# Kernel optimization log

Hardware: AMD Instinct MI355X
Metric: run time of the kernel (lower is better)

## Reference

```python
import jax, jax.numpy as jnp
import numpy as np
import math

E = 1024      # hidden_dim = embed_dim (num_heads=1 so head_dim=E)
ND = 512      # output_dim = asymmetric value dim
N_DOMAIN = 2048
LN_EPS = 1e-5
SCALE = math.sqrt(1.0 / E) * 2.0 * math.log(N_DOMAIN)


def layernorm(x, g, b):
    mu = jnp.mean(x, axis=-1, keepdims=True)
    var = jnp.var(x, axis=-1, keepdims=True)
    return (x - mu) * jax.lax.rsqrt(var + LN_EPS) * g + b


def setup_inputs() -> dict:
    key = jax.random.key(0)
    ks = jax.random.split(key, 5)
    B, L = 8, 2048
    return {
        "x": jax.random.normal(ks[0], (B, L, E), dtype=jnp.float32),
        "in_proj_w": jax.random.normal(ks[1], (2 * E + ND, E), dtype=jnp.float32) * 0.02,
        "w1": jax.random.normal(ks[2], (2048, ND), dtype=jnp.float32) * 0.02,
        "b1": jnp.zeros((2048,), dtype=jnp.float32),
        "w2": jax.random.normal(ks[3], (ND, 2048), dtype=jnp.float32) * 0.02,
        "b2": jnp.zeros((ND,), dtype=jnp.float32),
        "g1": jnp.ones((ND,), dtype=jnp.float32),
        "be1": jnp.zeros((ND,), dtype=jnp.float32),
        "g2": jnp.ones((ND,), dtype=jnp.float32),
        "be2": jnp.zeros((ND,), dtype=jnp.float32),
    }


def reference(x, in_proj_w, w1, b1, w2, b2, g1, be1, g2, be2):
    # fused in-projection (no bias): q,k get E dims, v gets ND dims
    proj = jnp.einsum("ble,fe->blf", x, in_proj_w)
    q = proj[..., :E]
    k = proj[..., E:2 * E]
    v = proj[..., 2 * E:]
    # custom scale: sqrt(1/head_dim) * 2 * log(N)
    scores = jnp.einsum("bld,bsd->bls", q * SCALE, k)  # [B, L, S]
    attn_w = jax.nn.softmax(scores, axis=-1)
    attn_out = jnp.einsum("bls,bsd->bld", attn_w, v)   # [B, L, ND] (no out proj)
    # skip=False (hidden_dim != output_dim): norm1(attn) only
    h = layernorm(attn_out, g1, be1)
    ff = jnp.einsum("bld,fd->blf", h, w1) + b1
    ff = jnp.einsum("blf,df->bld", jax.nn.relu(ff), w2) + b2
    return layernorm(h + ff, g2, be2)
```

## Files before the change

### kernel.cpp

```cpp
#include <hip/hip_runtime.h>
#include <hip/hip_bf16.h>

typedef unsigned short u16;
typedef unsigned int u32;
typedef float f32x4 __attribute__((ext_vector_type(4)));
typedef _Float16 f16x8 __attribute__((ext_vector_type(8)));
typedef u32 u32x4 __attribute__((ext_vector_type(4)));
typedef u32 u32x2 __attribute__((ext_vector_type(2)));

#define SEQ 2048
#define EDIM 1024

__device__ __forceinline__ u16 f2h(float f) {
  _Float16 h = (_Float16)f;
  return __builtin_bit_cast(u16, h);
}
__device__ __forceinline__ float h2f(u16 u) {
  return (float)__builtin_bit_cast(_Float16, u);
}
__device__ __forceinline__ u32 pk(float a, float b) {
  return (u32)f2h(a) | ((u32)f2h(b) << 16);
}

__global__ __launch_bounds__(256) void cvt_f16(const float* __restrict__ in,
                                               u16* __restrict__ out, int n8) {
  int i = blockIdx.x * 256 + threadIdx.x;
  if (i >= n8) return;
  const f32x4* p = (const f32x4*)(in + (size_t)i * 8);
  f32x4 a = p[0], b = p[1];
  u32x4 o = {pk(a[0], a[1]), pk(a[2], a[3]), pk(b[0], b[1]), pk(b[2], b[3])};
  *(u32x4*)(out + (size_t)i * 8) = o;
}

struct GemmP {
  const u16* A; const u16* B;
  int lda, ldb, K;
  long bsA, bsB, bsC;
  float* Cf; int ldc;
  u16* Cb;
  const float* bias;
  const u16* resid;
  u16* qk; u16* vT;
  float scale;
};

template <int EPI>
__global__ __launch_bounds__(512, 2) void gemm256(GemmP p) {
  __shared__ __align__(16) char lds[131072];
  const int tid = threadIdx.x;
  const int lane = tid & 63;
  const int wave = tid >> 6;
  const int wm = wave >> 2, wn = wave & 3;
  const int bn0 = blockIdx.x * 256;
  const int bm0 = blockIdx.y * 256;
  const int z = blockIdx.z;
  const u16* Ab = p.A + (long)z * p.bsA + (long)bm0 * p.lda;
  const u16* Bb = p.B + (long)z * p.bsB + (long)bn0 * p.ldb;

  const int ch0 = tid, ch1 = tid + 512;
  const int r0 = ch0 >> 2, s0 = ch0 & 3;
  const int r1 = ch1 >> 2, s1 = ch1 & 3;
  const long srcA0 = (long)r0 * p.lda + ((s0 ^ ((r0 >> 1) & 3)) << 3);
  const long srcA1 = (long)r1 * p.lda + ((s1 ^ ((r1 >> 1) & 3)) << 3);
  const long srcB0 = (long)r0 * p.ldb + ((s0 ^ ((r0 >> 1) & 3)) << 3);
  const long srcB1 = (long)r1 * p.ldb + ((s1 ^ ((r1 >> 1) & 3)) << 3);

  auto stage = [&](int s) {
    const int base = (s & 3) * 32768;
    const int k0 = s * 32;
    __builtin_amdgcn_global_load_lds(
        (const __attribute__((address_space(1))) u32*)(Ab + k0 + srcA0),
        (__attribute__((address_space(3))) u32*)(lds + base + ch0 * 16), 16, 0, 0);
    __builtin_amdgcn_global_load_lds(
        (const __attribute__((address_space(1))) u32*)(Ab + k0 + srcA1),
        (__attribute__((address_space(3))) u32*)(lds + base + ch1 * 16), 16, 0, 0);
    __builtin_amdgcn_global_load_lds(
        (const __attribute__((address_space(1))) u32*)(Bb + k0 + srcB0),
        (__attribute__((address_space(3))) u32*)(lds + base + 16384 + ch0 * 16), 16, 0, 0);
    __builtin_amdgcn_global_load_lds(
        (const __attribute__((address_space(1))) u32*)(Bb + k0 + srcB1),
        (__attribute__((address_space(3))) u32*)(lds + base + 16384 + ch1 * 16), 16, 0, 0);
  };

  int aoff[8], boff[4];
#pragma unroll
  for (int m = 0; m < 8; ++m) {
    int r = wm * 128 + m * 16 + (lane & 15);
    aoff[m] = r * 64 + ((((lane >> 4)) ^ ((r >> 1) & 3)) << 4);
  }
#pragma unroll
  for (int n = 0; n < 4; ++n) {
    int r = wn * 64 + n * 16 + (lane & 15);
    boff[n] = 16384 + r * 64 + ((((lane >> 4)) ^ ((r >> 1) & 3)) << 4);
  }

  f32x4 acc[8][4] = {};

  stage(0); stage(1); stage(2);
  asm volatile("s_waitcnt vmcnt(8)" ::: "memory");
  __builtin_amdgcn_s_barrier();
  asm volatile("" ::: "memory");

  const int NS = p.K >> 5;
  for (int s = 0; s < NS; ++s) {
    if (s + 3 < NS) stage(s + 3);
    const char* base = lds + (s & 3) * 32768;
    f16x8 av[8], bv[4];
#pragma unroll
    for (int m = 0; m < 8; ++m) av[m] = *(const f16x8*)(base + aoff[m]);
#pragma unroll
    for (int n = 0; n < 4; ++n) bv[n] = *(const f16x8*)(base + boff[n]);
    __builtin_amdgcn_s_setprio(1);
#pragma unroll
    for (int m = 0; m < 8; ++m)
#pragma unroll
      for (int n = 0; n < 4; ++n)
        acc[m][n] = __builtin_amdgcn_mfma_f32_16x16x32_f16(av[m], bv[n], acc[m][n], 0, 0, 0);
    __builtin_amdgcn_s_setprio(0);
    __builtin_amdgcn_sched_barrier(0);
    if (s + 3 < NS) {
      asm volatile("s_waitcnt vmcnt(8)" ::: "memory");
    } else if (s + 2 < NS) {
      asm volatile("s_waitcnt vmcnt(4)" ::: "memory");
    } else if (s + 1 < NS) {
      asm volatile("s_waitcnt vmcnt(0)" ::: "memory");
    }
    __builtin_amdgcn_s_barrier();
    asm volatile("" ::: "memory");
  }

#pragma unroll
  for (int i = 0; i < 8; ++i) {
#pragma unroll
    for (int j = 0; j < 4; ++j) {
      int mb = bm0 + wm * 128 + i * 16 + ((lane >> 4) << 2);
      int n = bn0 + wn * 64 + j * 16 + (lane & 15);
      if constexpr (EPI == 0) {
        float* dst = p.Cf + (long)z * p.bsC + (long)mb * p.ldc + n;
#pragma unroll
        for (int r = 0; r < 4; ++r) dst[(long)r * p.ldc] = acc[i][j][r];
      } else if constexpr (EPI == 1) {
        int b = mb >> 11, l0 = mb & 2047;
        if (n < EDIM) {
          u16* dst = p.qk + (long)b * 4194304 + (long)l0 * 1024 + n;
#pragma unroll
          for (int r = 0; r < 4; ++r) dst[r * 1024] = f2h(acc[i][j][r] * p.scale);
        } else if (n < 2 * EDIM) {
          u16* dst = p.qk + (long)b * 4194304 + 2097152 + (long)l0 * 1024 + (n - EDIM);
#pragma unroll
          for (int r = 0; r < 4; ++r) dst[r * 1024] = f2h(acc[i][j][r]);
        } else {
          u16* dst = p.vT + (long)b * 1048576 + (long)(n - 2 * EDIM) * 2048 + l0;
          u32x2 w = {pk(acc[i][j][0], acc[i][j][1]), pk(acc[i][j][2], acc[i][j][3])};
          *(u32x2*)dst = w;
        }
      } else if constexpr (EPI == 2) {
        u16* dst = p.Cb + (long)mb * p.ldc + n;
        float bias = p.bias[n];
#pragma unroll
        for (int r = 0; r < 4; ++r) dst[(long)r * p.ldc] = f2h(fmaxf(acc[i][j][r] + bias, 0.f));
      }
    }
  }
}

template <int EPI>
__global__ __launch_bounds__(256) void gemm_bt(GemmP p) {
  __shared__ __align__(16) char lds[32768];
  const int tid = threadIdx.x;
  const int lane = tid & 63;
  const int wave = tid >> 6;
  const int wm = wave >> 1, wn = wave & 1;
  const int bn0 = blockIdx.x * 128;
  const int bm0 = blockIdx.y * 128;
  const int z = blockIdx.z;
  const u16* Ab = p.A + (long)z * p.bsA + (long)bm0 * p.lda;
  const u16* Bb = p.B + (long)z * p.bsB + (long)bn0 * p.ldb;

  auto stage = [&](int k0) {
#pragma unroll
    for (int i = 0; i < 4; ++i) {
      int ch = i * 256 + tid;
      int row = ch >> 3, s = ch & 7;
      int ks = ((s ^ (row & 7)) << 3);
      __builtin_amdgcn_global_load_lds(
          (const __attribute__((address_space(1))) u32*)(Ab + (long)row * p.lda + k0 + ks),
          (__attribute__((address_space(3))) u32*)(lds + ch * 16), 16, 0, 0);
    }
#pragma unroll
    for (int i = 0; i < 4; ++i) {
      int ch = i * 256 + tid;
      int row = ch >> 3, s = ch & 7;
      int ks = ((s ^ (row & 7)) << 3);
      __builtin_amdgcn_global_load_lds(
          (const __attribute__((address_space(1))) u32*)(Bb + (long)row * p.ldb + k0 + ks),
          (__attribute__((address_space(3))) u32*)(lds + 16384 + ch * 16), 16, 0, 0);
    }
  };

  f32x4 acc[4][4] = {};
  stage(0);
  const int nk = p.K >> 6;
  for (int kt = 0; kt < nk; ++kt) {
    __syncthreads();
#pragma unroll
    for (int h = 0; h < 2; ++h) {
      f16x8 av[4], bv[4];
#pragma unroll
      for (int i = 0; i < 4; ++i) {
        int row = wm * 64 + i * 16 + (lane & 15);
        int sw = ((h << 2) | (lane >> 4)) ^ (lane & 7);
        av[i] = *(const f16x8*)(lds + row * 128 + sw * 16);
      }
#pragma unroll
      for (int j = 0; j < 4; ++j) {
        int row = wn * 64 + j * 16 + (lane & 15);
        int sw = ((h << 2) | (lane >> 4)) ^ (lane & 7);
        bv[j] = *(const f16x8*)(lds + 16384 + row * 128 + sw * 16);
      }
#pragma unroll
      for (int i = 0; i < 4; ++i)
#pragma unroll
        for (int j = 0; j < 4; ++j)
          acc[i][j] = __builtin_amdgcn_mfma_f32_16x16x32_f16(av[i], bv[j], acc[i][j], 0, 0, 0);
    }
    __syncthreads();
    if (kt + 1 < nk) stage((kt + 1) << 6);
  }

#pragma unroll
  for (int i = 0; i < 4; ++i) {
#pragma unroll
    for (int j = 0; j < 4; ++j) {
      int mb = bm0 + wm * 64 + i * 16 + ((lane >> 4) << 2);
      int n = bn0 + wn * 64 + j * 16 + (lane & 15);
      if constexpr (EPI == 0) {
        float* dst = p.Cf + (long)z * p.bsC + (long)mb * p.ldc + n;
#pragma unroll
        for (int r = 0; r < 4; ++r) dst[(long)r * p.ldc] = acc[i][j][r];
      } else {
        float bias = p.bias[n];
        float* dst = p.Cf + (long)mb * 512 + n;
        const u16* rs = p.resid + (long)mb * 512 + n;
#pragma unroll
        for (int r = 0; r < 4; ++r) dst[r * 512] = acc[i][j][r] + bias + h2f(rs[r * 512]);
      }
    }
  }
}

__global__ __launch_bounds__(256) void softmax_rows(const float* __restrict__ S,
                                                    u16* __restrict__ W, int b0) {
  int r = blockIdx.x;
  int z = r >> 11, l = r & 2047;
  int tid = threadIdx.x, lane = tid & 63, wv = tid >> 6;
  const float* x = S + (long)r * 2048 + tid * 8;
  f32x4 a = *(const f32x4*)x, b = *(const f32x4*)(x + 4);
  float m = fmaxf(fmaxf(fmaxf(a[0], a[1]), fmaxf(a[2], a[3])),
                  fmaxf(fmaxf(b[0], b[1]), fmaxf(b[2], b[3])));
#pragma unroll
  for (int off = 32; off; off >>= 1) m = fmaxf(m, __shfl_xor(m, off));
  __shared__ float red[8];
  if (lane == 0) red[wv] = m;
  __syncthreads();
  m = fmaxf(fmaxf(red[0], red[1]), fmaxf(red[2], red[3]));
  float e[8];
  float s = 0.f;
#pragma unroll
  for (int q = 0; q < 4; ++q) { e[q] = __expf(a[q] - m); s += e[q]; }
#pragma unroll
  for (int q = 0; q < 4; ++q) { e[4 + q] = __expf(b[q] - m); s += e[4 + q]; }
#pragma unroll
  for (int off = 32; off; off >>= 1) s += __shfl_xor(s, off);
  if (lane == 0) red[4 + wv] = s;
  __syncthreads();
  s = red[4] + red[5] + red[6] + red[7];
  float inv = 1.f / s;
  u32x4 o = {pk(e[0] * inv, e[1] * inv), pk(e[2] * inv, e[3] * inv),
             pk(e[4] * inv, e[5] * inv), pk(e[6] * inv, e[7] * inv)};
  *(u32x4*)(W + (long)(b0 + z) * 4194304 + (long)l * 2048 + tid * 8) = o;
}

template <int OUTF16>
__global__ __launch_bounds__(256) void ln_rows(const float* __restrict__ X,
                                               const float* __restrict__ g,
                                               const float* __restrict__ bb,
                                               void* __restrict__ out) {
  int row = blockIdx.x * 4 + (threadIdx.x >> 6);
  int lane = threadIdx.x & 63;
  const float* x = X + (long)row * 512 + lane * 8;
  f32x4 a = *(const f32x4*)x, b = *(const f32x4*)(x + 4);
  float s = a[0] + a[1] + a[2] + a[3] + b[0] + b[1] + b[2] + b[3];
  float sq = a[0] * a[0] + a[1] * a[1] + a[2] * a[2] + a[3] * a[3] +
             b[0] * b[0] + b[1] * b[1] + b[2] * b[2] + b[3] * b[3];
#pragma unroll
  for (int off = 32; off; off >>= 1) {
    s += __shfl_xor(s, off);
    sq += __shfl_xor(sq, off);
  }
  float mean = s * (1.f / 512.f);
  float var = sq * (1.f / 512.f) - mean * mean;
  float rstd = rsqrtf(var + 1e-5f);
  f32x4 g0 = *(const f32x4*)(g + lane * 8), g1v = *(const f32x4*)(g + lane * 8 + 4);
  f32x4 b0 = *(const f32x4*)(bb + lane * 8), b1v = *(const f32x4*)(bb + lane * 8 + 4);
  float o[8];
#pragma unroll
  for (int q = 0; q < 4; ++q) o[q] = (a[q] - mean) * rstd * g0[q] + b0[q];
#pragma unroll
  for (int q = 0; q < 4; ++q) o[4 + q] = (b[q] - mean) * rstd * g1v[q] + b1v[q];
  if constexpr (OUTF16) {
    u32x4 pkd = {pk(o[0], o[1]), pk(o[2], o[3]), pk(o[4], o[5]), pk(o[6], o[7])};
    *(u32x4*)((u16*)out + (long)row * 512 + lane * 8) = pkd;
  } else {
    float* dst = (float*)out + (long)row * 512 + lane * 8;
    *(f32x4*)dst = (f32x4){o[0], o[1], o[2], o[3]};
    *(f32x4*)(dst + 4) = (f32x4){o[4], o[5], o[6], o[7]};
  }
}

extern "C" void kernel_launch(void* const* d_in, const int* in_sizes, int n_in,
                              void* d_out, int out_size, void* d_ws, size_t ws_size,
                              hipStream_t stream) {
  const float* x = (const float*)d_in[0];
  const float* wp = (const float*)d_in[1];
  const float* w1 = (const float*)d_in[2];
  const float* b1 = (const float*)d_in[3];
  const float* w2 = (const float*)d_in[4];
  const float* b2 = (const float*)d_in[5];
  const float* g1 = (const float*)d_in[6];
  const float* be1 = (const float*)d_in[7];
  const float* g2 = (const float*)d_in[8];
  const float* be2 = (const float*)d_in[9];

  char* ws = (char*)d_ws;
  size_t off = 0;
  auto alloc = [&](size_t bytes) {
    char* p = ws + off;
    off += (bytes + 255) & ~(size_t)255;
    return p;
  };
  u16* wpb = (u16*)alloc(2560 * 1024 * 2);
  u16* w1b = (u16*)alloc(2048 * 512 * 2);
  u16* w2b = (u16*)alloc(512 * 2048 * 2);
  char* xb_region = alloc(33554432);
  u16* qk = (u16*)alloc(67108864);
  u16* vT = (u16*)alloc(16777216);
  u16* hb = (u16*)alloc(16777216);
  size_t remain = (ws_size > off) ? ws_size - off : 0;
  int bpl = (remain >= (size_t)67108864 + 256) ? 4 : 2;
  char* sc_region = alloc((size_t)bpl * 2048 * 2048 * 4);
  if (off > ws_size) return;

  u16* xb = (u16*)xb_region;
  float* attn_f = (float*)xb_region;
  float* scores = (float*)sc_region;
  float* y32 = (float*)sc_region;
  u16* ff1 = qk;

  const float SC = (float)(0.03125 * 2.0 * 7.6246189861593985);

  cvt_f16<<<dim3(8192), dim3(256), 0, stream>>>(x, xb, 2097152);
  cvt_f16<<<dim3(1280), dim3(256), 0, stream>>>(wp, wpb, 327680);
  cvt_f16<<<dim3(512), dim3(256), 0, stream>>>(w1, w1b, 131072);
  cvt_f16<<<dim3(512), dim3(256), 0, stream>>>(w2, w2b, 131072);

  {
    GemmP p{};
    p.A = xb; p.lda = 1024; p.B = wpb; p.ldb = 1024; p.K = 1024;
    p.qk = qk; p.vT = vT; p.scale = SC;
    gemm256<1><<<dim3(10, 64, 1), 512, 0, stream>>>(p);
  }

  for (int it = 0; it < 8 / bpl; ++it) {
    int b0 = it * bpl;
    GemmP p{};
    p.A = qk + (long)b0 * 4194304; p.lda = 1024; p.bsA = 4194304;
    p.B = qk + (long)b0 * 4194304 + 2097152; p.ldb = 1024; p.bsB = 4194304;
    p.K = 1024; p.Cf = scores; p.ldc = 2048; p.bsC = 4194304;
    gemm256<0><<<dim3(8, 8, bpl), 512, 0, stream>>>(p);
    softmax_rows<<<dim3(bpl * 2048), dim3(256), 0, stream>>>(scores, qk, b0);
  }

  {
    GemmP p{};
    p.A = qk; p.lda = 2048; p.bsA = 4194304;
    p.B = vT; p.ldb = 2048; p.bsB = 1048576;
    p.K = 2048; p.Cf = attn_f; p.ldc = 512; p.bsC = 1048576;
    gemm_bt<0><<<dim3(4, 16, 8), 256, 0, stream>>>(p);
  }

  ln_rows<1><<<dim3(4096), dim3(256), 0, stream>>>(attn_f, g1, be1, hb);

  {
    GemmP p{};
    p.A = hb; p.lda = 512; p.B = w1b; p.ldb = 512; p.K = 512;
    p.Cb = ff1; p.ldc = 2048; p.bias = b1;
    gemm256<2><<<dim3(8, 64, 1), 512, 0, stream>>>(p);
  }

  {
    GemmP p{};
    p.A = ff1; p.lda = 2048; p.B = w2b; p.ldb = 2048; p.K = 2048;
    p.Cf = y32; p.bias = b2; p.resid = hb;
    gemm_bt<3><<<dim3(4, 128, 1), 256, 0, stream>>>(p);
  }

  ln_rows<0><<<dim3(4096), dim3(256), 0, stream>>>(y32, g2, be2, (float*)d_out);
}
```

Baseline: 424.8 us.

## Split GEMM main loop into two barrier-separated MFMA phases with staggered prefetch

Splits the f16 MFMA GEMM k-loop into two halves. Each half first issues its LDS fragment reads and one half of the next-stage global-to-LDS prefetch (the A tile or the B tile), then runs 16 MFMAs at raised priority. Extra s_barrier and lgkmcnt waits bracket each phase so waves stay in step, aiming to overlap LDS reads and global loads with matrix work. The cost is four barriers per k-step instead of one, which can add stalls if the waves do not interleave as intended.

```diff
diff --git a/kernel.cpp b/kernel.cpp
--- a/kernel.cpp
+++ b/kernel.cpp
@@ -65,7 +65,7 @@
   const long srcB0 = (long)r0 * p.ldb + ((s0 ^ ((r0 >> 1) & 3)) << 3);
   const long srcB1 = (long)r1 * p.ldb + ((s1 ^ ((r1 >> 1) & 3)) << 3);
 
-  auto stage = [&](int s) {
+  auto stageA = [&](int s) {
     const int base = (s & 3) * 32768;
     const int k0 = s * 32;
     __builtin_amdgcn_global_load_lds(
@@ -74,6 +74,10 @@
     __builtin_amdgcn_global_load_lds(
         (const __attribute__((address_space(1))) u32*)(Ab + k0 + srcA1),
         (__attribute__((address_space(3))) u32*)(lds + base + ch1 * 16), 16, 0, 0);
+  };
+  auto stageB = [&](int s) {
+    const int base = (s & 3) * 32768;
+    const int k0 = s * 32;
     __builtin_amdgcn_global_load_lds(
         (const __attribute__((address_space(1))) u32*)(Bb + k0 + srcB0),
         (__attribute__((address_space(3))) u32*)(lds + base + 16384 + ch0 * 16), 16, 0, 0);
@@ -96,28 +100,54 @@
 
   f32x4 acc[8][4] = {};
 
-  stage(0); stage(1); stage(2);
+  stageA(0); stageB(0); stageA(1); stageB(1); stageA(2); stageB(2);
   asm volatile("s_waitcnt vmcnt(8)" ::: "memory");
   __builtin_amdgcn_s_barrier();
   asm volatile("" ::: "memory");
 
   const int NS = p.K >> 5;
   for (int s = 0; s < NS; ++s) {
-    if (s + 3 < NS) stage(s + 3);
     const char* base = lds + (s & 3) * 32768;
-    f16x8 av[8], bv[4];
-#pragma unroll
-    for (int m = 0; m < 8; ++m) av[m] = *(const f16x8*)(base + aoff[m]);
-#pragma unroll
-    for (int n = 0; n < 4; ++n) bv[n] = *(const f16x8*)(base + boff[n]);
+
+    f16x8 av0 = *(const f16x8*)(base + aoff[0]);
+    f16x8 av1 = *(const f16x8*)(base + aoff[1]);
+    f16x8 av2 = *(const f16x8*)(base + aoff[2]);
+    f16x8 av3 = *(const f16x8*)(base + aoff[3]);
+    f16x8 bv0 = *(const f16x8*)(base + boff[0]);
+    f16x8 bv1 = *(const f16x8*)(base + boff[1]);
+    f16x8 bv2 = *(const f16x8*)(base + boff[2]);
+    f16x8 bv3 = *(const f16x8*)(base + boff[3]);
+    if (s + 3 < NS) stageA(s + 3);
+    asm volatile("" ::: "memory");
+    __builtin_amdgcn_s_barrier();
+    asm volatile("s_waitcnt lgkmcnt(0)" ::: "memory");
+    __builtin_amdgcn_sched_barrier(0);
     __builtin_amdgcn_s_setprio(1);
-#pragma unroll
-    for (int m = 0; m < 8; ++m)
-#pragma unroll
-      for (int n = 0; n < 4; ++n)
-        acc[m][n] = __builtin_amdgcn_mfma_f32_16x16x32_f16(av[m], bv[n], acc[m][n], 0, 0, 0);
+    acc[0][0] = __builtin_amdgcn_mfma_f32_16x16x32_f16(av0, bv0, acc[0][0], 0, 0, 0);
+    acc[0][1] = __builtin_amdgcn_mfma_f32_16x16x32_f16(av0, bv1, acc[0][1], 0, 0, 0);
+    acc[0][2] = __builtin_amdgcn_mfma_f32_16x16x32_f16(av0, bv2, acc[0][2], 0, 0, 0);
+    acc[0][3] = __builtin_amdgcn_mfma_f32_16x16x32_f16(av0, bv3, acc[0][3], 0, 0, 0);
+    acc[1][0] = __builtin_amdgcn_mfma_f32_16x16x32_f16(av1, bv0, acc[1][0], 0, 0, 0);
+    acc[1][1] = __builtin_amdgcn_mfma_f32_16x16x32_f16(av1, bv1, acc[1][1], 0, 0, 0);
+    acc[1][2] = __builtin_amdgcn_mfma_f32_16x16x32_f16(av1, bv2, acc[1][2], 0, 0, 0);
+    acc[1][3] = __builtin_amdgcn_mfma_f32_16x16x32_f16(av1, bv3, acc[1][3], 0, 0, 0);
+    acc[2][0] = __builtin_amdgcn_mfma_f32_16x16x32_f16(av2, bv0, acc[2][0], 0, 0, 0);
+    acc[2][1] = __builtin_amdgcn_mfma_f32_16x16x32_f16(av2, bv1, acc[2][1], 0, 0, 0);
+    acc[2][2] = __builtin_amdgcn_mfma_f32_16x16x32_f16(av2, bv2, acc[2][2], 0, 0, 0);
+    acc[2][3] = __builtin_amdgcn_mfma_f32_16x16x32_f16(av2, bv3, acc[2][3], 0, 0, 0);
+    acc[3][0] = __builtin_amdgcn_mfma_f32_16x16x32_f16(av3, bv0, acc[3][0], 0, 0, 0);
+    acc[3][1] = __builtin_amdgcn_mfma_f32_16x16x32_f16(av3, bv1, acc[3][1], 0, 0, 0);
+    acc[3][2] = __builtin_amdgcn_mfma_f32_16x16x32_f16(av3, bv2, acc[3][2], 0, 0, 0);
+    acc[3][3] = __builtin_amdgcn_mfma_f32_16x16x32_f16(av3, bv3, acc[3][3], 0, 0, 0);
     __builtin_amdgcn_s_setprio(0);
-    __builtin_amdgcn_sched_barrier(0);
+    asm volatile("" ::: "memory");
+    __builtin_amdgcn_s_barrier();
+
+    f16x8 av4 = *(const f16x8*)(base + aoff[4]);
+    f16x8 av5 = *(const f16x8*)(base + aoff[5]);
+    f16x8 av6 = *(const f16x8*)(base + aoff[6]);
+    f16x8 av7 = *(const f16x8*)(base + aoff[7]);
+    if (s + 3 < NS) stageB(s + 3);
     if (s + 3 < NS) {
       asm volatile("s_waitcnt vmcnt(8)" ::: "memory");
     } else if (s + 2 < NS) {
@@ -126,7 +156,28 @@
       asm volatile("s_waitcnt vmcnt(0)" ::: "memory");
     }
     __builtin_amdgcn_s_barrier();
+    asm volatile("s_waitcnt lgkmcnt(0)" ::: "memory");
+    __builtin_amdgcn_sched_barrier(0);
+    __builtin_amdgcn_s_setprio(1);
+    acc[4][0] = __builtin_amdgcn_mfma_f32_16x16x32_f16(av4, bv0, acc[4][0], 0, 0, 0);
+    acc[4][1] = __builtin_amdgcn_mfma_f32_16x16x32_f16(av4, bv1, acc[4][1], 0, 0, 0);
+    acc[4][2] = __builtin_amdgcn_mfma_f32_16x16x32_f16(av4, bv2, acc[4][2], 0, 0, 0);
+    acc[4][3] = __builtin_amdgcn_mfma_f32_16x16x32_f16(av4, bv3, acc[4][3], 0, 0, 0);
+    acc[5][0] = __builtin_amdgcn_mfma_f32_16x16x32_f16(av5, bv0, acc[5][0], 0, 0, 0);
+    acc[5][1] = __builtin_amdgcn_mfma_f32_16x16x32_f16(av5, bv1, acc[5][1], 0, 0, 0);
+    acc[5][2] = __builtin_amdgcn_mfma_f32_16x16x32_f16(av5, bv2, acc[5][2], 0, 0, 0);
+    acc[5][3] = __builtin_amdgcn_mfma_f32_16x16x32_f16(av5, bv3, acc[5][3], 0, 0, 0);
+    acc[6][0] = __builtin_amdgcn_mfma_f32_16x16x32_f16(av6, bv0, acc[6][0], 0, 0, 0);
+    acc[6][1] = __builtin_amdgcn_mfma_f32_16x16x32_f16(av6, bv1, acc[6][1], 0, 0, 0);
+    acc[6][2] = __builtin_amdgcn_mfma_f32_16x16x32_f16(av6, bv2, acc[6][2], 0, 0, 0);
+    acc[6][3] = __builtin_amdgcn_mfma_f32_16x16x32_f16(av6, bv3, acc[6][3], 0, 0, 0);
+    acc[7][0] = __builtin_amdgcn_mfma_f32_16x16x32_f16(av7, bv0, acc[7][0], 0, 0, 0);
+    acc[7][1] = __builtin_amdgcn_mfma_f32_16x16x32_f16(av7, bv1, acc[7][1], 0, 0, 0);
+    acc[7][2] = __builtin_amdgcn_mfma_f32_16x16x32_f16(av7, bv2, acc[7][2], 0, 0, 0);
+    acc[7][3] = __builtin_amdgcn_mfma_f32_16x16x32_f16(av7, bv3, acc[7][3], 0, 0, 0);
+    __builtin_amdgcn_s_setprio(0);
     asm volatile("" ::: "memory");
+    __builtin_amdgcn_s_barrier();
   }
 
 #pragma unroll
```

New measurement: 428.3 us. About the same (+0.8%).
